# Kernel optimization log

Hardware: AMD Instinct MI355X
Metric: run time of the kernel (lower is better)

The kernel has to match this reference:

```python
import jax, jax.numpy as jnp
import numpy as np

B, T, HID = 8, 4, 2048
H, HKV, D = 32, 8, 64   # query heads, kv heads, head_dim
S = 8192                # cached kv length
EPS = 1e-6
SCALE = D ** -0.5


def _rmsnorm(x, w, eps=EPS):
    xf = x.astype(jnp.float32)
    var = jnp.mean(xf * xf, axis=-1, keepdims=True)
    return w * (xf * jax.lax.rsqrt(var + eps)).astype(x.dtype)


def _rotate_half(x):
    half = x.shape[-1] // 2
    return jnp.concatenate([-x[..., half:], x[..., :half]], axis=-1)


def setup_inputs() -> dict:
    key = jax.random.key(0)
    ks = jax.random.split(key, 12)
    f = jnp.float32
    x = jax.random.normal(ks[0], (B, T, HID), f)
    theta = jax.random.uniform(ks[1], (B, T, D), f, 0.0, 2.0 * np.pi)
    cos = jnp.cos(theta)
    sin = jnp.sin(theta)
    cache_keys = jax.random.normal(ks[2], (B, HKV, S, D), f) * 0.5
    cache_values = jax.random.normal(ks[3], (B, HKV, S, D), f) * 0.5
    wq = jax.random.normal(ks[4], (HID, H * D), f) * 0.02
    wk = jax.random.normal(ks[5], (HID, HKV * D), f) * 0.02
    wv = jax.random.normal(ks[6], (HID, HKV * D), f) * 0.02
    wo = jax.random.normal(ks[7], (H * D, HID), f) * 0.02
    q_norm_w = jnp.ones((D,), f)
    k_norm_w = jnp.ones((D,), f)
    return {"x": x, "cos": cos, "sin": sin, "cache_keys": cache_keys,
            "cache_values": cache_values, "wq": wq, "wk": wk, "wv": wv,
            "wo": wo, "q_norm_w": q_norm_w, "k_norm_w": k_norm_w}


def reference(x, cos, sin, cache_keys, cache_values, wq, wk, wv, wo, q_norm_w, k_norm_w):
    b, t, _ = x.shape
    # projections + per-head RMSNorm on q/k -> [B,H,T,D]
    q = _rmsnorm((x @ wq).reshape(b, t, H, D), q_norm_w).transpose(0, 2, 1, 3)
    k = _rmsnorm((x @ wk).reshape(b, t, HKV, D), k_norm_w).transpose(0, 2, 1, 3)
    v = (x @ wv).reshape(b, t, HKV, D).transpose(0, 2, 1, 3)
    # RoPE (GPT-NeoX style), cos/sin broadcast over heads
    c = cos[:, None]  # [B,1,T,D]
    s = sin[:, None]
    q = q * c + _rotate_half(q) * s
    k = k * c + _rotate_half(k) * s
    # KV-cache concat along seq dim
    k_full = jnp.concatenate([cache_keys, k], axis=2)   # [B,HKV,S+T,D]
    v_full = jnp.concatenate([cache_values, v], axis=2)
    # GQA attention without materializing repeated KV heads:
    n_rep = H // HKV
    qg = q.reshape(b, HKV, n_rep, t, D)                 # [B,G,R,T,D]
    scores = jnp.einsum('bgrtd,bgsd->bgrts', qg, k_full) * SCALE
    p = jax.nn.softmax(scores, axis=-1)                 # cache present -> no causal mask
    og = jnp.einsum('bgrts,bgsd->bgrtd', p, v_full)
    out = og.reshape(b, H, t, D).transpose(0, 2, 1, 3).reshape(b, t, H * D) @ wo
    return (out, k_full, v_full)
```

## Files before the change

kernel.cpp:

```cpp
#include <hip/hip_runtime.h>
#include <math.h>

#define B 8
#define T 4
#define HID 2048
#define H 32
#define HKV 8
#define D 64
#define S 8192
#define ST (S + T)
#define NREP (H / HKV)
#define EPS 1e-6f
#define SCALE 0.125f

#define GM 32
#define SCB 256
#define SUB 64
#define NCB 33

typedef __attribute__((ext_vector_type(8))) _Float16 half8;
typedef __attribute__((ext_vector_type(4))) _Float16 half4;
typedef __attribute__((ext_vector_type(4))) float f32x4;

#define LGKM_BARRIER()                                                   \
    do {                                                                 \
        asm volatile("s_waitcnt lgkmcnt(0)" ::: "memory");               \
        __builtin_amdgcn_s_barrier();                                    \
        __builtin_amdgcn_sched_barrier(0);                               \
    } while (0)

static __device__ __forceinline__ half8 cvt8(const float4 a, const float4 b) {
    half8 f;
    f[0] = (_Float16)a.x; f[1] = (_Float16)a.y; f[2] = (_Float16)a.z; f[3] = (_Float16)a.w;
    f[4] = (_Float16)b.x; f[5] = (_Float16)b.y; f[6] = (_Float16)b.z; f[7] = (_Float16)b.w;
    return f;
}
static __device__ __forceinline__ half4 cvt4v(const f32x4 a) {
    half4 f;
    f[0] = (_Float16)a[0]; f[1] = (_Float16)a[1]; f[2] = (_Float16)a[2]; f[3] = (_Float16)a[3];
    return f;
}

__global__ __launch_bounds__(256) void zero2(float4* __restrict__ a, int na,
                                             float4* __restrict__ b, int nb) {
    const float4 z = {0.f, 0.f, 0.f, 0.f};
    int i = blockIdx.x * 256 + threadIdx.x;
    const int n = na + nb;
    for (; i < n; i += gridDim.x * 256) {
        if (i < na) a[i] = z; else b[i - na] = z;
    }
}

__global__ __launch_bounds__(256) void gemm_qkv(const float* __restrict__ x,
                                                const float* __restrict__ wq,
                                                const float* __restrict__ wk,
                                                const float* __restrict__ wv,
                                                float* __restrict__ q_raw,
                                                float* __restrict__ k_raw,
                                                float* __restrict__ v_raw) {
    __shared__ float xs[128][36];
    const int tid = threadIdx.x;
    const int k0 = blockIdx.y * 128;
    const int tile = blockIdx.x;

    const float* w; float* y; int N, colbase;
    if (tile < 16)      { w = wq; y = q_raw; N = 2048; colbase = tile * 128; }
    else if (tile < 20) { w = wk; y = k_raw; N = 512;  colbase = (tile - 16) * 128; }
    else                { w = wv; y = v_raw; N = 512;  colbase = (tile - 20) * 128; }

    for (int j = tid; j < 32 * 32; j += 256) {
        const int m = j >> 5;
        const int kk = (j & 31) * 4;
        const float4 xv = *(const float4*)&x[(size_t)m * HID + k0 + kk];
        xs[kk + 0][m] = xv.x; xs[kk + 1][m] = xv.y;
        xs[kk + 2][m] = xv.z; xs[kk + 3][m] = xv.w;
    }
    __syncthreads();

    const int ksub = tid & 3, cid = tid >> 2;
    const int col0 = colbase + cid;
    const int col1 = col0 + 64;
    float acc0[GM], acc1[GM];
#pragma unroll
    for (int m = 0; m < GM; ++m) { acc0[m] = 0.f; acc1[m] = 0.f; }

    for (int ii = 0; ii < 32; ++ii) {
        const int kl_ = ksub * 32 + ii;
        const float w0 = w[(size_t)(k0 + kl_) * N + col0];
        const float w1 = w[(size_t)(k0 + kl_) * N + col1];
#pragma unroll
        for (int m4 = 0; m4 < GM; m4 += 4) {
            const float4 xv = *(const float4*)&xs[kl_][m4];
            acc0[m4 + 0] += xv.x * w0; acc1[m4 + 0] += xv.x * w1;
            acc0[m4 + 1] += xv.y * w0; acc1[m4 + 1] += xv.y * w1;
            acc0[m4 + 2] += xv.z * w0; acc1[m4 + 2] += xv.z * w1;
            acc0[m4 + 3] += xv.w * w0; acc1[m4 + 3] += xv.w * w1;
        }
    }
#pragma unroll
    for (int m = 0; m < GM; ++m) {
        acc0[m] += __shfl_xor(acc0[m], 1); acc0[m] += __shfl_xor(acc0[m], 2);
        acc1[m] += __shfl_xor(acc1[m], 1); acc1[m] += __shfl_xor(acc1[m], 2);
    }
    if (ksub == 0) {
#pragma unroll
        for (int m = 0; m < GM; ++m) {
            atomicAdd(&y[(size_t)m * N + col0], acc0[m]);
            atomicAdd(&y[(size_t)m * N + col1], acc1[m]);
        }
    }
}

__global__ __launch_bounds__(256) void gemm_v2(const float* __restrict__ x, int ldx,
                                               const float* __restrict__ w, int N,
                                               float* __restrict__ y) {
    __shared__ float xs[128][36];
    const int tid = threadIdx.x;
    const int k0 = blockIdx.y * 128;

    for (int j = tid; j < 32 * 32; j += 256) {
        const int m = j >> 5;
        const int kk = (j & 31) * 4;
        const float4 xv = *(const float4*)&x[(size_t)m * ldx + k0 + kk];
        xs[kk + 0][m] = xv.x; xs[kk + 1][m] = xv.y;
        xs[kk + 2][m] = xv.z; xs[kk + 3][m] = xv.w;
    }
    __syncthreads();

    const int ksub = tid & 3, cid = tid >> 2;
    const int col0 = blockIdx.x * 128 + cid;
    const int col1 = col0 + 64;
    float acc0[GM], acc1[GM];
#pragma unroll
    for (int m = 0; m < GM; ++m) { acc0[m] = 0.f; acc1[m] = 0.f; }

    for (int ii = 0; ii < 32; ++ii) {
        const int kl_ = ksub * 32 + ii;
        const float w0 = w[(size_t)(k0 + kl_) * N + col0];
        const float w1 = w[(size_t)(k0 + kl_) * N + col1];
#pragma unroll
        for (int m4 = 0; m4 < GM; m4 += 4) {
            const float4 xv = *(const float4*)&xs[kl_][m4];
            acc0[m4 + 0] += xv.x * w0; acc1[m4 + 0] += xv.x * w1;
            acc0[m4 + 1] += xv.y * w0; acc1[m4 + 1] += xv.y * w1;
            acc0[m4 + 2] += xv.z * w0; acc1[m4 + 2] += xv.z * w1;
            acc0[m4 + 3] += xv.w * w0; acc1[m4 + 3] += xv.w * w1;
        }
    }
#pragma unroll
    for (int m = 0; m < GM; ++m) {
        acc0[m] += __shfl_xor(acc0[m], 1); acc0[m] += __shfl_xor(acc0[m], 2);
        acc1[m] += __shfl_xor(acc1[m], 1); acc1[m] += __shfl_xor(acc1[m], 2);
    }
    if (ksub == 0) {
#pragma unroll
        for (int m = 0; m < GM; ++m) {
            atomicAdd(&y[(size_t)m * N + col0], acc0[m]);
            atomicAdd(&y[(size_t)m * N + col1], acc1[m]);
        }
    }
}

__global__ __launch_bounds__(256) void qkv_post(const float* __restrict__ q_raw,
                                                const float* __restrict__ k_raw,
                                                const float* __restrict__ v_raw,
                                                const float* __restrict__ cosb,
                                                const float* __restrict__ sinb,
                                                const float* __restrict__ qnw,
                                                const float* __restrict__ knw,
                                                float* __restrict__ q_fin,
                                                float* __restrict__ kfull,
                                                float* __restrict__ vfull) {
    const int wid = (blockIdx.x * 256 + threadIdx.x) >> 6;
    const int lane = threadIdx.x & 63;
    if (wid < 1024) {
        const int m = wid >> 5, h = wid & 31;
        float v = q_raw[(size_t)m * 2048 + h * 64 + lane];
        float ss = v * v;
#pragma unroll
        for (int off = 32; off; off >>= 1) ss += __shfl_xor(ss, off);
        float nv = qnw[lane] * v * rsqrtf(ss * (1.f / 64.f) + EPS);
        float other = __shfl_xor(nv, 32);
        float rot = (lane < 32) ? -other : other;
        float outv = nv * cosb[m * 64 + lane] + rot * sinb[m * 64 + lane];
        q_fin[(size_t)m * 2048 + h * 64 + lane] = outv * SCALE;
    } else if (wid < 1280) {
        const int idx = wid - 1024;
        const int m = idx >> 3, g = idx & 7;
        float v = k_raw[(size_t)m * 512 + g * 64 + lane];
        float ss = v * v;
#pragma unroll
        for (int off = 32; off; off >>= 1) ss += __shfl_xor(ss, off);
        float nv = knw[lane] * v * rsqrtf(ss * (1.f / 64.f) + EPS);
        float other = __shfl_xor(nv, 32);
        float rot = (lane < 32) ? -other : other;
        float outv = nv * cosb[m * 64 + lane] + rot * sinb[m * 64 + lane];
        const int b = m >> 2, t = m & 3;
        kfull[((size_t)(b * HKV + g) * ST + S + t) * D + lane] = outv;
    } else if (wid < 1536) {
        const int idx = wid - 1280;
        const int m = idx >> 3, g = idx & 7;
        float v = v_raw[(size_t)m * 512 + g * 64 + lane];
        const int b = m >> 2, t = m & 3;
        vfull[((size_t)(b * HKV + g) * ST + S + t) * D + lane] = v;
    }
}

__global__ __launch_bounds__(256, 5) void attn_part(const float* __restrict__ q_fin,
                                                    const float* __restrict__ ck,
                                                    const float* __restrict__ cv,
                                                    float* __restrict__ kfull,
                                                    float* __restrict__ vfull,
                                                    float* __restrict__ o_part,
                                                    float* __restrict__ ml_part) {
    const int bg = blockIdx.x;
    const int cb = blockIdx.y;
    const int b = bg >> 3, g = bg & 7;
    const int tid = threadIdx.x;
    const int lane = tid & 63;
    const int w = tid >> 6;
    const int q16 = lane & 15;
    const int kgrp = lane >> 4;

    __shared__ __align__(16) _Float16 kl[SUB][72];
    __shared__ __align__(16) _Float16 vl[SUB][72];
    __shared__ __align__(16) float scs[16][68];
    __shared__ __align__(16) _Float16 pb[16][72];
    __shared__ float Mrun[16], Lrun[16], srow[16];

    const bool full = (cb < 32);
    const int vm1 = full ? (SUB - 1) : (ST - S - 1);

    if (tid < 16) { Mrun[tid] = -3e38f; Lrun[tid] = 0.f; }

    half8 qf[2];
    {
        const float* qp = q_fin + ((size_t)(b * T + (q16 & 3)) * H + g * NREP + (q16 >> 2)) * D;
#pragma unroll
        for (int h = 0; h < 2; ++h) {
            const float* p = qp + h * 32 + kgrp * 8;
            qf[h] = cvt8(*(const float4*)p, *(const float4*)(p + 4));
        }
    }

    f32x4 oacc = {0.f, 0.f, 0.f, 0.f};
    const int dglob = w * 16 + q16;

    if (full) {
        const f32x4* ksrc = (const f32x4*)(ck + ((size_t)bg * S + (size_t)cb * SCB) * D);
        const f32x4* vsrc = (const f32x4*)(cv + ((size_t)bg * S + (size_t)cb * SCB) * D);
        f32x4* kdst = (f32x4*)(kfull + ((size_t)bg * ST + (size_t)cb * SCB) * D);
        f32x4* vdst = (f32x4*)(vfull + ((size_t)bg * ST + (size_t)cb * SCB) * D);

        f32x4 kr[4], vr[4];
#pragma unroll
        for (int i = 0; i < 4; ++i) {
            kr[i] = __builtin_nontemporal_load(&ksrc[tid + i * 256]);
            vr[i] = __builtin_nontemporal_load(&vsrc[tid + i * 256]);
        }

#pragma unroll
        for (int su = 0; su < 4; ++su) {
#pragma unroll
            for (int i = 0; i < 4; ++i) {
                const int idx = tid + i * 256;
                __builtin_nontemporal_store(kr[i], &kdst[su * 1024 + idx]);
                __builtin_nontemporal_store(vr[i], &vdst[su * 1024 + idx]);
                const int r = idx >> 4, cg = idx & 15;
                *(half4*)&kl[r][cg * 4] = cvt4v(kr[i]);
                *(half4*)&vl[r][cg * 4] = cvt4v(vr[i]);
            }
            if (su < 3) {
#pragma unroll
                for (int i = 0; i < 4; ++i) {
                    kr[i] = __builtin_nontemporal_load(&ksrc[(su + 1) * 1024 + tid + i * 256]);
                    vr[i] = __builtin_nontemporal_load(&vsrc[(su + 1) * 1024 + tid + i * 256]);
                }
            }
            LGKM_BARRIER();

            {
                const int sl = w * 16 + q16;
                f32x4 acc = {0.f, 0.f, 0.f, 0.f};
#pragma unroll
                for (int h = 0; h < 2; ++h) {
                    const half8 kf = *(const half8*)&kl[sl][h * 32 + kgrp * 8];
                    acc = __builtin_amdgcn_mfma_f32_16x16x32_f16(kf, qf[h], acc, 0, 0, 0);
                }
                *(f32x4*)&scs[q16][w * 16 + kgrp * 4] = acc;
            }
            LGKM_BARRIER();

#pragma unroll
            for (int rr = 0; rr < 4; ++rr) {
                const int row = w * 4 + rr;
                const float v = scs[row][lane];
                float m_ = v;
#pragma unroll
                for (int off = 32; off; off >>= 1) m_ = fmaxf(m_, __shfl_xor(m_, off));
                const float Mold = Mrun[row];
                const float Mnew = fmaxf(Mold, m_);
                const float e = __expf(v - Mnew);
                float l = e;
#pragma unroll
                for (int off = 32; off; off >>= 1) l += __shfl_xor(l, off);
                pb[row][lane] = (_Float16)e;
                if (lane == 0) {
                    const float sc_ = __expf(Mold - Mnew);
                    srow[row] = sc_;
                    Lrun[row] = Lrun[row] * sc_ + l;
                    Mrun[row] = Mnew;
                }
            }
            LGKM_BARRIER();

            {
#pragma unroll
                for (int r = 0; r < 4; ++r) oacc[r] *= srow[kgrp * 4 + r];
#pragma unroll
                for (int ks = 0; ks < 2; ++ks) {
                    const half8 pa = *(const half8*)&pb[q16][ks * 32 + kgrp * 8];
                    half8 vf;
#pragma unroll
                    for (int e = 0; e < 8; ++e) {
                        vf[e] = vl[ks * 32 + kgrp * 8 + e][dglob];
                    }
                    oacc = __builtin_amdgcn_mfma_f32_16x16x32_f16(pa, vf, oacc, 0, 0, 0);
                }
            }
            LGKM_BARRIER();
        }
    } else {
        if (tid < 64) {
            const int r = tid >> 4, cg = tid & 15;
            const int rc = min(r, vm1);
            const f32x4 k4 = *(const f32x4*)(kfull + ((size_t)bg * ST + S + rc) * D + cg * 4);
            const f32x4 v4 = *(const f32x4*)(vfull + ((size_t)bg * ST + S + rc) * D + cg * 4);
            *(half4*)&kl[r][cg * 4] = cvt4v(k4);
            *(half4*)&vl[r][cg * 4] = cvt4v(v4);
        }
        __syncthreads();

        {
            const int sl = min(w * 16 + q16, vm1);
            f32x4 acc = {0.f, 0.f, 0.f, 0.f};
#pragma unroll
            for (int h = 0; h < 2; ++h) {
                const half8 kf = *(const half8*)&kl[sl][h * 32 + kgrp * 8];
                acc = __builtin_amdgcn_mfma_f32_16x16x32_f16(kf, qf[h], acc, 0, 0, 0);
            }
            const int sbase = w * 16 + kgrp * 4;
#pragma unroll
            for (int r = 0; r < 4; ++r)
                scs[q16][sbase + r] = (sbase + r <= vm1) ? acc[r] : -1e30f;
        }
        __syncthreads();

#pragma unroll
        for (int rr = 0; rr < 4; ++rr) {
            const int row = w * 4 + rr;
            const float v = scs[row][lane];
            float m_ = v;
#pragma unroll
            for (int off = 32; off; off >>= 1) m_ = fmaxf(m_, __shfl_xor(m_, off));
            const float Mnew = m_;
            const float e = __expf(v - Mnew);
            float l = e;
#pragma unroll
            for (int off = 32; off; off >>= 1) l += __shfl_xor(l, off);
            pb[row][lane] = (_Float16)e;
            if (lane == 0) { srow[row] = 0.f; Lrun[row] = l; Mrun[row] = Mnew; }
        }
        __syncthreads();

        {
#pragma unroll
            for (int ks = 0; ks < 2; ++ks) {
                const half8 pa = *(const half8*)&pb[q16][ks * 32 + kgrp * 8];
                half8 vf;
#pragma unroll
                for (int e = 0; e < 8; ++e) {
                    const int sr = min(ks * 32 + kgrp * 8 + e, vm1);
                    vf[e] = vl[sr][dglob];
                }
                oacc = __builtin_amdgcn_mfma_f32_16x16x32_f16(pa, vf, oacc, 0, 0, 0);
            }
        }
        __syncthreads();
    }

#pragma unroll
    for (int r = 0; r < 4; ++r) {
        const int row = kgrp * 4 + r;
        o_part[(((size_t)bg * 16 + row) * NCB + cb) * 64 + dglob] = oacc[r];
    }
    if (tid < 16) {
        ml_part[(((size_t)bg * 16 + tid) * NCB + cb) * 2 + 0] = Mrun[tid];
        ml_part[(((size_t)bg * 16 + tid) * NCB + cb) * 2 + 1] = Lrun[tid];
    }
}

__global__ __launch_bounds__(256) void attn_combine(const float* __restrict__ o_part,
                                                    const float* __restrict__ ml_part,
                                                    float* __restrict__ og) {
    const int gw = (blockIdx.x * 256 + threadIdx.x) >> 6;
    const int lane = threadIdx.x & 63;
    const int bg = gw >> 4, row = gw & 15;
    float M = -1e30f, L = 0.f, O = 0.f;
    for (int c = 0; c < NCB; ++c) {
        const float m_ = ml_part[((size_t)gw * NCB + c) * 2 + 0];
        const float l_ = ml_part[((size_t)gw * NCB + c) * 2 + 1];
        const float o_ = o_part[((size_t)gw * NCB + c) * 64 + lane];
        const float Mn = fmaxf(M, m_);
        const float fa = __expf(M - Mn), fb = __expf(m_ - Mn);
        O = O * fa + o_ * fb;
        L = L * fa + l_ * fb;
        M = Mn;
    }
    const float o = O / L;
    const int b = bg >> 3, g = bg & 7, r = row >> 2, t = row & 3;
    og[((size_t)(b * T + t) * H + (g * NREP + r)) * D + lane] = o;
}

extern "C" void kernel_launch(void* const* d_in, const int* in_sizes, int n_in,
                              void* d_out, int out_size, void* d_ws, size_t ws_size,
                              hipStream_t stream) {
    const float* x    = (const float*)d_in[0];
    const float* cosb = (const float*)d_in[1];
    const float* sinb = (const float*)d_in[2];
    const float* ck   = (const float*)d_in[3];
    const float* cv   = (const float*)d_in[4];
    const float* wq   = (const float*)d_in[5];
    const float* wk   = (const float*)d_in[6];
    const float* wvp  = (const float*)d_in[7];
    const float* wo   = (const float*)d_in[8];
    const float* qnw  = (const float*)d_in[9];
    const float* knw  = (const float*)d_in[10];

    float* out   = (float*)d_out;
    float* kfull = out + 65536;
    float* vfull = kfull + (size_t)B * HKV * ST * D;

    float* ws      = (float*)d_ws;
    float* q_raw   = ws;
    float* k_raw   = q_raw + 65536;
    float* v_raw   = k_raw + 16384;
    float* q_fin   = v_raw + 16384;
    float* og      = q_fin + 65536;
    float* o_part  = og + 65536;
    float* ml_part = o_part + (size_t)64 * 16 * NCB * 64;

    zero2<<<160, 256, 0, stream>>>((float4*)q_raw, 98304 / 4, (float4*)out, 65536 / 4);

    gemm_qkv<<<dim3(24, 16), 256, 0, stream>>>(x, wq, wk, wvp, q_raw, k_raw, v_raw);

    qkv_post<<<384, 256, 0, stream>>>(q_raw, k_raw, v_raw, cosb, sinb, qnw, knw,
                                      q_fin, kfull, vfull);

    attn_part<<<dim3(64, NCB), 256, 0, stream>>>(q_fin, ck, cv, kfull, vfull, o_part, ml_part);

    attn_combine<<<256, 256, 0, stream>>>(o_part, ml_part, og);

    gemm_v2<<<dim3(2048 / 128, 16), 256, 0, stream>>>(og, 2048, wo, 2048, out);
}
```

Measured before the change: 162.3 us.

## Replace scalar split-K projection GEMMs with fp16 MFMA kernels and drop zeroing launch

Rewrites the QKV and output projection GEMMs to use 16x16x32 fp16 MFMA instructions. Inputs and weights are converted to half in shared memory, and split-K is reduced from 16 to 2. QKV partial sums are written to a two-slice buffer that qkv_post adds together, which removes the atomics and the separate zeroing kernel. The output buffer is now zeroed inside attn_combine. This trades fp32 precision for matrix-core throughput and also cuts kernel launches. The risks are lower accuracy and less parallelism from using fewer blocks.

New measurement: 150.6 us. -7.2%, faster.

```diff
diff --git a/kernel.cpp b/kernel.cpp
--- a/kernel.cpp
+++ b/kernel.cpp
@@ -13,10 +13,11 @@
 #define EPS 1e-6f
 #define SCALE 0.125f
 
-#define GM 32
 #define SCB 256
+#define NSUB 4
 #define SUB 64
 #define NCB 33
+#define NCAT 3072
 
 typedef __attribute__((ext_vector_type(8))) _Float16 half8;
 typedef __attribute__((ext_vector_type(4))) _Float16 half4;
@@ -41,129 +42,125 @@
     return f;
 }
 
-__global__ __launch_bounds__(256) void zero2(float4* __restrict__ a, int na,
-                                             float4* __restrict__ b, int nb) {
-    const float4 z = {0.f, 0.f, 0.f, 0.f};
-    int i = blockIdx.x * 256 + threadIdx.x;
-    const int n = na + nb;
-    for (; i < n; i += gridDim.x * 256) {
-        if (i < na) a[i] = z; else b[i - na] = z;
-    }
-}
-
-__global__ __launch_bounds__(256) void gemm_qkv(const float* __restrict__ x,
-                                                const float* __restrict__ wq,
-                                                const float* __restrict__ wk,
-                                                const float* __restrict__ wv,
-                                                float* __restrict__ q_raw,
-                                                float* __restrict__ k_raw,
-                                                float* __restrict__ v_raw) {
-    __shared__ float xs[128][36];
+__global__ __launch_bounds__(256) void gemm_qkv_mfma(const float* __restrict__ x,
+                                                     const float* __restrict__ wq,
+                                                     const float* __restrict__ wk,
+                                                     const float* __restrict__ wv,
+                                                     float* __restrict__ part) {
+    __shared__ __align__(16) _Float16 xs[32][136];
+    __shared__ __align__(16) _Float16 wsl[32][136];
+
     const int tid = threadIdx.x;
-    const int k0 = blockIdx.y * 128;
+    const int lane = tid & 63;
+    const int w = tid >> 6;
+    const int q16 = lane & 15;
+    const int kgrp = lane >> 4;
     const int tile = blockIdx.x;
-
-    const float* w; float* y; int N, colbase;
-    if (tile < 16)      { w = wq; y = q_raw; N = 2048; colbase = tile * 128; }
-    else if (tile < 20) { w = wk; y = k_raw; N = 512;  colbase = (tile - 16) * 128; }
-    else                { w = wv; y = v_raw; N = 512;  colbase = (tile - 20) * 128; }
-
-    for (int j = tid; j < 32 * 32; j += 256) {
-        const int m = j >> 5;
-        const int kk = (j & 31) * 4;
-        const float4 xv = *(const float4*)&x[(size_t)m * HID + k0 + kk];
-        xs[kk + 0][m] = xv.x; xs[kk + 1][m] = xv.y;
-        xs[kk + 2][m] = xv.z; xs[kk + 3][m] = xv.w;
-    }
-    __syncthreads();
-
-    const int ksub = tid & 3, cid = tid >> 2;
-    const int col0 = colbase + cid;
-    const int col1 = col0 + 64;
-    float acc0[GM], acc1[GM];
-#pragma unroll
-    for (int m = 0; m < GM; ++m) { acc0[m] = 0.f; acc1[m] = 0.f; }
-
-    for (int ii = 0; ii < 32; ++ii) {
-        const int kl_ = ksub * 32 + ii;
-        const float w0 = w[(size_t)(k0 + kl_) * N + col0];
-        const float w1 = w[(size_t)(k0 + kl_) * N + col1];
-#pragma unroll
-        for (int m4 = 0; m4 < GM; m4 += 4) {
-            const float4 xv = *(const float4*)&xs[kl_][m4];
-            acc0[m4 + 0] += xv.x * w0; acc1[m4 + 0] += xv.x * w1;
-            acc0[m4 + 1] += xv.y * w0; acc1[m4 + 1] += xv.y * w1;
-            acc0[m4 + 2] += xv.z * w0; acc1[m4 + 2] += xv.z * w1;
-            acc0[m4 + 3] += xv.w * w0; acc1[m4 + 3] += xv.w * w1;
-        }
-    }
-#pragma unroll
-    for (int m = 0; m < GM; ++m) {
-        acc0[m] += __shfl_xor(acc0[m], 1); acc0[m] += __shfl_xor(acc0[m], 2);
-        acc1[m] += __shfl_xor(acc1[m], 1); acc1[m] += __shfl_xor(acc1[m], 2);
-    }
-    if (ksub == 0) {
-#pragma unroll
-        for (int m = 0; m < GM; ++m) {
-            atomicAdd(&y[(size_t)m * N + col0], acc0[m]);
-            atomicAdd(&y[(size_t)m * N + col1], acc1[m]);
-        }
-    }
-}
-
-__global__ __launch_bounds__(256) void gemm_v2(const float* __restrict__ x, int ldx,
-                                               const float* __restrict__ w, int N,
-                                               float* __restrict__ y) {
-    __shared__ float xs[128][36];
+    const int ky = blockIdx.y;
+    const int kbase = ky * 1024;
+
+    const float* wsrc; int N, lcbase;
+    if (tile < 64)      { wsrc = wq; N = 2048; lcbase = tile * 32; }
+    else if (tile < 80) { wsrc = wk; N = 512;  lcbase = (tile - 64) * 32; }
+    else                { wsrc = wv; N = 512;  lcbase = (tile - 80) * 32; }
+
+    const int r0 = (w >> 1) * 16, c0 = (w & 1) * 16;
+    f32x4 acc = {0.f, 0.f, 0.f, 0.f};
+
+    for (int kc = 0; kc < 8; ++kc) {
+        const int k0 = kbase + kc * 128;
+#pragma unroll
+        for (int i = 0; i < 4; ++i) {
+            const int idx = tid + i * 256;
+            const int m = idx >> 5, slot = idx & 31;
+            const f32x4 xv = *(const f32x4*)&x[(size_t)m * HID + k0 + slot * 4];
+            *(half4*)&xs[m][slot * 4] = cvt4v(xv);
+        }
+#pragma unroll
+        for (int i = 0; i < 4; ++i) {
+            const int idx = tid + i * 256;
+            const int kk = idx >> 3, c4 = idx & 7;
+            const f32x4 wv4 = *(const f32x4*)&wsrc[(size_t)(k0 + kk) * N + lcbase + c4 * 4];
+            wsl[c4 * 4 + 0][kk] = (_Float16)wv4[0];
+            wsl[c4 * 4 + 1][kk] = (_Float16)wv4[1];
+            wsl[c4 * 4 + 2][kk] = (_Float16)wv4[2];
+            wsl[c4 * 4 + 3][kk] = (_Float16)wv4[3];
+        }
+        __syncthreads();
+#pragma unroll
+        for (int ks = 0; ks < 4; ++ks) {
+            const half8 af = *(const half8*)&xs[r0 + q16][ks * 32 + kgrp * 8];
+            const half8 bf = *(const half8*)&wsl[c0 + q16][ks * 32 + kgrp * 8];
+            acc = __builtin_amdgcn_mfma_f32_16x16x32_f16(af, bf, acc, 0, 0, 0);
+        }
+        __syncthreads();
+    }
+
+    const int gcol = tile * 32 + c0 + q16;
+#pragma unroll
+    for (int r = 0; r < 4; ++r) {
+        const int m = r0 + kgrp * 4 + r;
+        part[((size_t)ky * 32 + m) * NCAT + gcol] = acc[r];
+    }
+}
+
+__global__ __launch_bounds__(256) void gemm_out_mfma(const float* __restrict__ og,
+                                                     const float* __restrict__ wo,
+                                                     float* __restrict__ out) {
+    __shared__ __align__(16) _Float16 xs[32][136];
+    __shared__ __align__(16) _Float16 wsl[32][136];
+
     const int tid = threadIdx.x;
-    const int k0 = blockIdx.y * 128;
-
-    for (int j = tid; j < 32 * 32; j += 256) {
-        const int m = j >> 5;
-        const int kk = (j & 31) * 4;
-        const float4 xv = *(const float4*)&x[(size_t)m * ldx + k0 + kk];
-        xs[kk + 0][m] = xv.x; xs[kk + 1][m] = xv.y;
-        xs[kk + 2][m] = xv.z; xs[kk + 3][m] = xv.w;
-    }
-    __syncthreads();
-
-    const int ksub = tid & 3, cid = tid >> 2;
-    const int col0 = blockIdx.x * 128 + cid;
-    const int col1 = col0 + 64;
-    float acc0[GM], acc1[GM];
-#pragma unroll
-    for (int m = 0; m < GM; ++m) { acc0[m] = 0.f; acc1[m] = 0.f; }
-
-    for (int ii = 0; ii < 32; ++ii) {
-        const int kl_ = ksub * 32 + ii;
-        const float w0 = w[(size_t)(k0 + kl_) * N + col0];
-        const float w1 = w[(size_t)(k0 + kl_) * N + col1];
-#pragma unroll
-        for (int m4 = 0; m4 < GM; m4 += 4) {
-            const float4 xv = *(const float4*)&xs[kl_][m4];
-            acc0[m4 + 0] += xv.x * w0; acc1[m4 + 0] += xv.x * w1;
-            acc0[m4 + 1] += xv.y * w0; acc1[m4 + 1] += xv.y * w1;
-            acc0[m4 + 2] += xv.z * w0; acc1[m4 + 2] += xv.z * w1;
-            acc0[m4 + 3] += xv.w * w0; acc1[m4 + 3] += xv.w * w1;
-        }
-    }
-#pragma unroll
-    for (int m = 0; m < GM; ++m) {
-        acc0[m] += __shfl_xor(acc0[m], 1); acc0[m] += __shfl_xor(acc0[m], 2);
-        acc1[m] += __shfl_xor(acc1[m], 1); acc1[m] += __shfl_xor(acc1[m], 2);
-    }
-    if (ksub == 0) {
-#pragma unroll
-        for (int m = 0; m < GM; ++m) {
-            atomicAdd(&y[(size_t)m * N + col0], acc0[m]);
-            atomicAdd(&y[(size_t)m * N + col1], acc1[m]);
-        }
-    }
-}
-
-__global__ __launch_bounds__(256) void qkv_post(const float* __restrict__ q_raw,
-                                                const float* __restrict__ k_raw,
-                                                const float* __restrict__ v_raw,
+    const int lane = tid & 63;
+    const int w = tid >> 6;
+    const int q16 = lane & 15;
+    const int kgrp = lane >> 4;
+    const int tile = blockIdx.x;
+    const int ky = blockIdx.y;
+    const int kbase = ky * 1024;
+    const int lcbase = tile * 32;
+
+    const int r0 = (w >> 1) * 16, c0 = (w & 1) * 16;
+    f32x4 acc = {0.f, 0.f, 0.f, 0.f};
+
+    for (int kc = 0; kc < 8; ++kc) {
+        const int k0 = kbase + kc * 128;
+#pragma unroll
+        for (int i = 0; i < 4; ++i) {
+            const int idx = tid + i * 256;
+            const int m = idx >> 5, slot = idx & 31;
+            const f32x4 xv = *(const f32x4*)&og[(size_t)m * 2048 + k0 + slot * 4];
+            *(half4*)&xs[m][slot * 4] = cvt4v(xv);
+        }
+#pragma unroll
+        for (int i = 0; i < 4; ++i) {
+            const int idx = tid + i * 256;
+            const int kk = idx >> 3, c4 = idx & 7;
+            const f32x4 wv4 = *(const f32x4*)&wo[(size_t)(k0 + kk) * 2048 + lcbase + c4 * 4];
+            wsl[c4 * 4 + 0][kk] = (_Float16)wv4[0];
+            wsl[c4 * 4 + 1][kk] = (_Float16)wv4[1];
+            wsl[c4 * 4 + 2][kk] = (_Float16)wv4[2];
+            wsl[c4 * 4 + 3][kk] = (_Float16)wv4[3];
+        }
+        __syncthreads();
+#pragma unroll
+        for (int ks = 0; ks < 4; ++ks) {
+            const half8 af = *(const half8*)&xs[r0 + q16][ks * 32 + kgrp * 8];
+            const half8 bf = *(const half8*)&wsl[c0 + q16][ks * 32 + kgrp * 8];
+            acc = __builtin_amdgcn_mfma_f32_16x16x32_f16(af, bf, acc, 0, 0, 0);
+        }
+        __syncthreads();
+    }
+
+    const int gcol = lcbase + c0 + q16;
+#pragma unroll
+    for (int r = 0; r < 4; ++r) {
+        const int m = r0 + kgrp * 4 + r;
+        atomicAdd(&out[(size_t)m * 2048 + gcol], acc[r]);
+    }
+}
+
+__global__ __launch_bounds__(256) void qkv_post(const float* __restrict__ part,
                                                 const float* __restrict__ cosb,
                                                 const float* __restrict__ sinb,
                                                 const float* __restrict__ qnw,
@@ -175,7 +172,8 @@
     const int lane = threadIdx.x & 63;
     if (wid < 1024) {
         const int m = wid >> 5, h = wid & 31;
-        float v = q_raw[(size_t)m * 2048 + h * 64 + lane];
+        const size_t c = (size_t)m * NCAT + h * 64 + lane;
+        float v = part[c] + part[c + (size_t)32 * NCAT];
         float ss = v * v;
 #pragma unroll
         for (int off = 32; off; off >>= 1) ss += __shfl_xor(ss, off);
@@ -187,7 +185,8 @@
     } else if (wid < 1280) {
         const int idx = wid - 1024;
         const int m = idx >> 3, g = idx & 7;
-        float v = k_raw[(size_t)m * 512 + g * 64 + lane];
+        const size_t c = (size_t)m * NCAT + 2048 + g * 64 + lane;
+        float v = part[c] + part[c + (size_t)32 * NCAT];
         float ss = v * v;
 #pragma unroll
         for (int off = 32; off; off >>= 1) ss += __shfl_xor(ss, off);
@@ -200,7 +199,8 @@
     } else if (wid < 1536) {
         const int idx = wid - 1280;
         const int m = idx >> 3, g = idx & 7;
-        float v = v_raw[(size_t)m * 512 + g * 64 + lane];
+        const size_t c = (size_t)m * NCAT + 2560 + g * 64 + lane;
+        float v = part[c] + part[c + (size_t)32 * NCAT];
         const int b = m >> 2, t = m & 3;
         vfull[((size_t)(b * HKV + g) * ST + S + t) * D + lane] = v;
     }
@@ -260,7 +260,7 @@
         }
 
 #pragma unroll
-        for (int su = 0; su < 4; ++su) {
+        for (int su = 0; su < NSUB; ++su) {
 #pragma unroll
             for (int i = 0; i < 4; ++i) {
                 const int idx = tid + i * 256;
@@ -270,7 +270,7 @@
                 *(half4*)&kl[r][cg * 4] = cvt4v(kr[i]);
                 *(half4*)&vl[r][cg * 4] = cvt4v(vr[i]);
             }
-            if (su < 3) {
+            if (su < NSUB - 1) {
 #pragma unroll
                 for (int i = 0; i < 4; ++i) {
                     kr[i] = __builtin_nontemporal_load(&ksrc[(su + 1) * 1024 + tid + i * 256]);
@@ -402,7 +402,10 @@
 
 __global__ __launch_bounds__(256) void attn_combine(const float* __restrict__ o_part,
                                                     const float* __restrict__ ml_part,
-                                                    float* __restrict__ og) {
+                                                    float* __restrict__ og,
+                                                    float* __restrict__ out) {
+    out[blockIdx.x * 256 + threadIdx.x] = 0.f;
+
     const int gw = (blockIdx.x * 256 + threadIdx.x) >> 6;
     const int lane = threadIdx.x & 63;
     const int bg = gw >> 4, row = gw & 15;
@@ -442,24 +445,19 @@
     float* vfull = kfull + (size_t)B * HKV * ST * D;
 
     float* ws      = (float*)d_ws;
-    float* q_raw   = ws;
-    float* k_raw   = q_raw + 65536;
-    float* v_raw   = k_raw + 16384;
-    float* q_fin   = v_raw + 16384;
+    float* qkvp    = ws;
+    float* q_fin   = qkvp + (size_t)2 * 32 * NCAT;
     float* og      = q_fin + 65536;
     float* o_part  = og + 65536;
     float* ml_part = o_part + (size_t)64 * 16 * NCB * 64;
 
-    zero2<<<160, 256, 0, stream>>>((float4*)q_raw, 98304 / 4, (float4*)out, 65536 / 4);
-
-    gemm_qkv<<<dim3(24, 16), 256, 0, stream>>>(x, wq, wk, wvp, q_raw, k_raw, v_raw);
-
-    qkv_post<<<384, 256, 0, stream>>>(q_raw, k_raw, v_raw, cosb, sinb, qnw, knw,
-                                      q_fin, kfull, vfull);
+    gemm_qkv_mfma<<<dim3(96, 2), 256, 0, stream>>>(x, wq, wk, wvp, qkvp);
+
+    qkv_post<<<384, 256, 0, stream>>>(qkvp, cosb, sinb, qnw, knw, q_fin, kfull, vfull);
 
     attn_part<<<dim3(64, NCB), 256, 0, stream>>>(q_fin, ck, cv, kfull, vfull, o_part, ml_part);
 
-    attn_combine<<<256, 256, 0, stream>>>(o_part, ml_part, og);
-
-    gemm_v2<<<dim3(2048 / 128, 16), 256, 0, stream>>>(og, 2048, wo, 2048, out);
-}
+    attn_combine<<<256, 256, 0, stream>>>(o_part, ml_part, og, out);
+
+    gemm_out_mfma<<<dim3(64, 2), 256, 0, stream>>>(og, wo, out);
+}
```
